# Kernel optimization log

Measured on AMD Instinct MI355X. Metric: run time of the kernel, lower is better.

The kernel has to match this reference:

```python
import jax, jax.numpy as jnp
import numpy as np

ACT_BITS = 8  # config.activation_bits
HIDDEN = 2048
INTERMEDIATE = 4096  # hidden * mlp_ratio (2.0), power of 2
EPS = 1e-5


def fwht(x):
    """Normalized fast Walsh-Hadamard transform along last axis (n = power of 2)."""
    shape = x.shape
    n = shape[-1]
    x = x.reshape(-1, n)
    h = 1
    while h < n:  # log2(n) fixed iterations, not a data-dim loop
        x = x.reshape(-1, n // (2 * h), 2, h)
        a, b = x[:, :, 0, :], x[:, :, 1, :]
        x = jnp.stack((a + b, a - b), axis=2).reshape(-1, n)
        h *= 2
    return (x * (1.0 / np.sqrt(n))).reshape(shape)


def _ste(x, q):
    # straight-through estimator: forward uses q, backward passes grad to x
    return x + jax.lax.stop_gradient(q - x)


def act_quant(x, bits):
    """Per-token absmax quantization to `bits` bits (BitNet a8 style), dequantized."""
    qb = float(2 ** (bits - 1) - 1)
    scale = qb / jnp.clip(jnp.max(jnp.abs(x), axis=-1, keepdims=True), EPS, None)
    q = jnp.clip(jnp.round(x * scale), -qb, qb) / scale
    return _ste(x, q)


def weight_quant(w):
    """Ternary absmean weight quantization (BitNet b1.58), dequantized."""
    scale = jnp.clip(jnp.mean(jnp.abs(w)), EPS, None)
    q = jnp.clip(jnp.round(w / scale), -1.0, 1.0) * scale
    return _ste(w, q)


def hbitlinear(x, w, bits):
    # H-BitLinear: Hadamard-rotate activations, quantize acts + weights, GEMM
    xq = act_quant(fwht(x), bits)
    wq = weight_quant(w)
    return jnp.einsum('bsd,fd->bsf', xq, wq)


def setup_inputs() -> dict:
    key = jax.random.key(0)
    k1, k2, k3 = jax.random.split(key, 3)
    hidden_states = jax.random.normal(k1, (4, 4096, HIDDEN), dtype=jnp.float32)
    w_up = jax.random.normal(k2, (INTERMEDIATE, HIDDEN), dtype=jnp.float32) * 0.02
    w_down = jax.random.normal(k3, (HIDDEN, INTERMEDIATE), dtype=jnp.float32) * 0.02
    return {"hidden_states": hidden_states, "w_up": w_up, "w_down": w_down}


def reference(hidden_states, w_up, w_down):
    h = hbitlinear(hidden_states, w_up, ACT_BITS)      # (B, S, intermediate)
    h = jnp.square(jax.nn.relu(h))                     # squared ReLU
    # dropout p=0.0 -> identity in eval/reference
    return hbitlinear(h, w_down, ACT_BITS)             # (B, S, hidden)
```

## Files before the change

### kernel.cpp

```cpp
#include <hip/hip_runtime.h>
#include <hip/hip_fp16.h>
#include <cstdint>
#include <cstddef>

#define HIDDEN 2048
#define INTER  4096
#define EPSQ   1e-5f

typedef int v4i __attribute__((ext_vector_type(4)));

__device__ __forceinline__ void async_ld16(const void* g, void* l) {
  __builtin_amdgcn_global_load_lds((const __attribute__((address_space(1))) void*)g,
                                   (__attribute__((address_space(3))) void*)l, 16, 0, 0);
}

#define BAR()   __builtin_amdgcn_s_barrier()
#define VMC(n)  asm volatile("s_waitcnt vmcnt(" #n ")" ::: "memory")

__global__ void absmean_kernel(const float* __restrict__ w, size_t n4, double* __restrict__ out) {
  double s = 0.0;
  const float4* w4 = (const float4*)w;
  for (size_t i = blockIdx.x * (size_t)blockDim.x + threadIdx.x; i < n4;
       i += (size_t)gridDim.x * blockDim.x) {
    float4 v = w4[i];
    s += (double)fabsf(v.x) + (double)fabsf(v.y) + (double)fabsf(v.z) + (double)fabsf(v.w);
  }
  #pragma unroll
  for (int o = 32; o; o >>= 1) s += __shfl_down(s, o);
  __shared__ double red[4];
  if ((threadIdx.x & 63) == 0) red[threadIdx.x >> 6] = s;
  __syncthreads();
  if (threadIdx.x == 0) atomicAdd(out, red[0] + red[1] + red[2] + red[3]);
}

__global__ void quantw_kernel(const float* __restrict__ w, size_t n4,
                              const double* __restrict__ sum, double invcnt,
                              int8_t* __restrict__ q) {
  const float scale = (float)fmax(sum[0] * invcnt, (double)EPSQ);
  const float4* w4 = (const float4*)w;
  char4* q4 = (char4*)q;
  for (size_t i = blockIdx.x * (size_t)blockDim.x + threadIdx.x; i < n4;
       i += (size_t)gridDim.x * blockDim.x) {
    float4 v = w4[i];
    char4 c;
    c.x = (signed char)fmaxf(-1.f, fminf(1.f, rintf(v.x / scale)));
    c.y = (signed char)fmaxf(-1.f, fminf(1.f, rintf(v.y / scale)));
    c.z = (signed char)fmaxf(-1.f, fminf(1.f, rintf(v.z / scale)));
    c.w = (signed char)fmaxf(-1.f, fminf(1.f, rintf(v.w / scale)));
    q4[i] = c;
  }
}

template <int LOGN, bool HALF_IN>
__global__ void __launch_bounds__(256) fwht_quant_kernel(const void* __restrict__ Xv,
                                                         int8_t* __restrict__ Q,
                                                         float* __restrict__ invs) {
  constexpr int N = 1 << LOGN;
  constexpr int E = N / 64;
  const int lane = threadIdx.x & 63;
  const size_t t = (size_t)blockIdx.x * 4 + (threadIdx.x >> 6);

  float r[E];
  if constexpr (HALF_IN) {
    const int4* xp = (const int4*)((const __half*)Xv + t * (size_t)N + lane * E);
    #pragma unroll
    for (int u = 0; u < E / 8; ++u) {
      alignas(16) __half hb[8];
      *(int4*)hb = xp[u];
      #pragma unroll
      for (int j = 0; j < 8; ++j) r[u * 8 + j] = __half2float(hb[j]);
    }
  } else {
    const float4* xp = (const float4*)((const float*)Xv + t * (size_t)N + lane * E);
    #pragma unroll
    for (int u = 0; u < E / 4; ++u) {
      float4 v = xp[u];
      r[u * 4 + 0] = v.x; r[u * 4 + 1] = v.y; r[u * 4 + 2] = v.z; r[u * 4 + 3] = v.w;
    }
  }

  #pragma unroll
  for (int m = 1; m < E; m <<= 1) {
    #pragma unroll
    for (int e = 0; e < E; ++e) {
      if (!(e & m)) {
        float a = r[e], b = r[e | m];
        r[e] = a + b;
        r[e | m] = a - b;
      }
    }
  }
  #pragma unroll
  for (int m = 1; m < 64; m <<= 1) {
    const float sgn = (lane & m) ? -1.f : 1.f;
    #pragma unroll
    for (int e = 0; e < E; ++e) {
      float w = __shfl_xor(r[e], m, 64);
      r[e] = fmaf(r[e], sgn, w);
    }
  }

  float mx = 0.f;
  #pragma unroll
  for (int e = 0; e < E; ++e) mx = fmaxf(mx, fabsf(r[e]));
  #pragma unroll
  for (int m = 1; m < 64; m <<= 1) mx = fmaxf(mx, __shfl_xor(mx, m, 64));

  constexpr float c = (LOGN == 11) ? 0.022097086912079608f : 0.015625f;
  mx = fmaxf(mx * c, EPSQ);
  const float sc = 127.0f * c / mx;
  if (lane == 0) invs[t] = mx * (1.0f / 127.0f);

  alignas(16) int8_t qv[E];
  #pragma unroll
  for (int e = 0; e < E; ++e) {
    float q = rintf(r[e] * sc);
    q = fmaxf(-127.f, fminf(127.f, q));
    qv[e] = (int8_t)q;
  }
  int8_t* qp = Q + t * (size_t)N + lane * E;
  #pragma unroll
  for (int u = 0; u < E / 16; ++u) ((int4*)qp)[u] = ((const int4*)qv)[u];
}

template <bool RELU2, typename TOUT>
__global__ __launch_bounds__(512, 2)
void gemm_i8_8ph(const int8_t* __restrict__ A, const int8_t* __restrict__ B,
                 TOUT* __restrict__ C, const float* __restrict__ invs,
                 const double* __restrict__ wsum, double invcnt,
                 int N, int K) {
  __shared__ int8_t As[2 * 2 * 128 * 128];
  __shared__ int8_t Bs[2 * 2 * 128 * 128];

  const int GX = N >> 8;
  const int nwg = gridDim.x;
  int wg = blockIdx.x;
  wg = (wg & 7) * (nwg >> 3) + (wg >> 3);
  const int bx = wg % GX;
  const int by = wg / GX;
  const int m0 = by * 256, n0 = bx * 256;

  const int t = threadIdx.x;
  const int lane = t & 63;
  const int wave = t >> 6;
  const int wr = wave >> 2;
  const int wc = wave & 3;

  const int row0 = t >> 3;
  const int colsw = ((t & 7) * 16) ^ ((row0 & 7) << 4);
  const int8_t* gA0 = A + (size_t)(m0 + row0) * K + colsw;
  const int8_t* gA1 = gA0 + (size_t)128 * K;
  const int8_t* gB0 = B + (size_t)(n0 + row0) * K + colsw;
  const int8_t* gB1 = gB0 + (size_t)128 * K;
  const size_t rstep = (size_t)64 * K;

  auto SA = [&](int bf, int hf, int kt) {
    const int8_t* g = (hf ? gA1 : gA0) + (size_t)kt * 128;
    int8_t* l = As + bf * 32768 + hf * 16384 + t * 16;
    async_ld16(g, l);
    async_ld16(g + rstep, l + 8192);
  };
  auto SB = [&](int bf, int hf, int kt) {
    const int8_t* g = (hf ? gB1 : gB0) + (size_t)kt * 128;
    int8_t* l = Bs + bf * 32768 + hf * 16384 + t * 16;
    async_ld16(g, l);
    async_ld16(g + rstep, l + 8192);
  };

  const int csw0 = ((lane >> 4) * 16) ^ ((lane & 7) << 4);
  const int csw1 = (64 + (lane >> 4) * 16) ^ ((lane & 7) << 4);
  const int8_t* pA0 = As + wr * 16384 + (lane & 15) * 128;
  const int8_t* pB0 = Bs + (wc >> 1) * 16384 + ((wc & 1) * 64 + (lane & 15)) * 128;

  v4i acc[8][4] = {};
  v4i a[4][2], b[4][2];

  auto RDA = [&](int bf, int m4) {
    const int8_t* p = pA0 + bf * 32768 + m4 * 8192;
    #pragma unroll
    for (int mt = 0; mt < 4; ++mt) {
      a[mt][0] = *(const v4i*)(p + mt * 2048 + csw0);
      a[mt][1] = *(const v4i*)(p + mt * 2048 + csw1);
    }
  };
  auto RDB = [&](int bf, int n2) {
    const int8_t* p = pB0 + bf * 32768 + n2 * 4096;
    #pragma unroll
    for (int nt = 0; nt < 2; ++nt) {
      b[n2 * 2 + nt][0] = *(const v4i*)(p + nt * 2048 + csw0);
      b[n2 * 2 + nt][1] = *(const v4i*)(p + nt * 2048 + csw1);
    }
  };
  auto MM = [&](int m4, int n2) {
    __builtin_amdgcn_s_setprio(1);
    #pragma unroll
    for (int mt = 0; mt < 4; ++mt)
      #pragma unroll
      for (int nt = 0; nt < 2; ++nt) {
        v4i* c = &acc[m4 * 4 + mt][n2 * 2 + nt];
        *c = __builtin_amdgcn_mfma_i32_16x16x64_i8(a[mt][0], b[n2 * 2 + nt][0], *c, 0, 0, 0);
        *c = __builtin_amdgcn_mfma_i32_16x16x64_i8(a[mt][1], b[n2 * 2 + nt][1], *c, 0, 0, 0);
      }
    __builtin_amdgcn_s_setprio(0);
  };

  const int NIT = K >> 8;

  SB(0, 0, 0); SB(0, 1, 0); SA(0, 0, 0); SA(0, 1, 0);
  SB(1, 0, 1); SB(1, 1, 1); SA(1, 0, 1); SA(1, 1, 1);
  VMC(8);
  BAR();

  for (int it = 0; it < NIT; ++it) {
    const int kt2 = 2 * it + 2, kt3 = 2 * it + 3;
    const bool more = it < NIT - 1;

    RDA(0, 0); RDB(0, 0);
    BAR(); MM(0, 0); BAR();

    RDB(0, 1);
    BAR(); MM(0, 1); BAR();

    RDA(0, 1);
    if (more) { SB(0, 0, kt2); SB(0, 1, kt2); }
    BAR(); MM(1, 0); BAR();

    if (more) { SA(0, 0, kt2); SA(0, 1, kt2); VMC(8); } else { VMC(0); }
    BAR(); MM(1, 1); BAR();

    RDA(1, 0); RDB(1, 0);
    BAR(); MM(0, 0); BAR();

    RDB(1, 1);
    BAR(); MM(0, 1); BAR();

    RDA(1, 1);
    if (more) { SB(1, 0, kt3); SB(1, 1, kt3); }
    BAR(); MM(1, 0); BAR();

    if (more) { SA(1, 0, kt3); SA(1, 1, kt3); VMC(8); }
    BAR(); MM(1, 1); BAR();
  }

  const float wscale = (float)fmax(wsum[0] * invcnt, (double)EPSQ);
  const int crow_base = m0 + wr * 128 + (lane >> 4) * 4;
  const int ccol_base = n0 + wc * 64 + (lane & 15);
  #pragma unroll
  for (int mt = 0; mt < 8; ++mt) {
    const int trow = crow_base + mt * 16;
    float fr[4];
    #pragma unroll
    for (int r = 0; r < 4; ++r) fr[r] = wscale * invs[trow + r];
    #pragma unroll
    for (int nt = 0; nt < 4; ++nt) {
      const int col = ccol_base + nt * 16;
      #pragma unroll
      for (int r = 0; r < 4; ++r) {
        float v = (float)acc[mt][nt][r] * fr[r];
        if (RELU2) v = v > 0.f ? v * v : 0.f;
        if constexpr (sizeof(TOUT) == 2)
          C[(size_t)(trow + r) * N + col] = __float2half(v);
        else
          C[(size_t)(trow + r) * N + col] = v;
      }
    }
  }
}

extern "C" void kernel_launch(void* const* d_in, const int* in_sizes, int n_in,
                              void* d_out, int out_size, void* d_ws, size_t ws_size,
                              hipStream_t stream) {
  const float* x      = (const float*)d_in[0];
  const float* w_up   = (const float*)d_in[1];
  const float* w_down = (const float*)d_in[2];
  float* out = (float*)d_out;

  const int T = in_sizes[0] / HIDDEN;
  const size_t WN = (size_t)INTER * HIDDEN;

  char* ws = (char*)d_ws;
  double* sums   = (double*)ws;
  float* invs1   = (float*)(ws + 256);
  float* invs2   = (float*)(ws + 256 + 65536);
  int8_t* wq_up  = (int8_t*)(ws + 131328);
  int8_t* wq_dn  = wq_up + WN;
  int8_t* a8_1   = wq_dn + WN;
  int8_t* a8_2   = a8_1 + (size_t)T * HIDDEN;
  __half* h      = (__half*)(a8_2 + (size_t)T * INTER);

  const double invcnt = 1.0 / (double)WN;

  hipMemsetAsync(sums, 0, 256, stream);
  absmean_kernel<<<1024, 256, 0, stream>>>(w_up, WN / 4, sums + 0);
  absmean_kernel<<<1024, 256, 0, stream>>>(w_down, WN / 4, sums + 1);
  quantw_kernel<<<2048, 256, 0, stream>>>(w_up, WN / 4, sums + 0, invcnt, wq_up);
  quantw_kernel<<<2048, 256, 0, stream>>>(w_down, WN / 4, sums + 1, invcnt, wq_dn);

  fwht_quant_kernel<11, false><<<T / 4, 256, 0, stream>>>(x, a8_1, invs1);
  gemm_i8_8ph<true, __half><<<(T / 256) * (INTER / 256), 512, 0, stream>>>(
      a8_1, wq_up, h, invs1, sums + 0, invcnt, INTER, HIDDEN);
  fwht_quant_kernel<12, true><<<T / 4, 256, 0, stream>>>(h, a8_2, invs2);
  gemm_i8_8ph<false, float><<<(T / 256) * (HIDDEN / 256), 512, 0, stream>>>(
      a8_2, wq_dn, out, invs2, sums + 1, invcnt, HIDDEN, INTER);
}
```

Measured before the change: 654.8 us.

## Software-pipeline LDS fragment reads with ping-pong registers and fewer barriers in int8 GEMM

```diff
diff --git a/kernel.cpp b/kernel.cpp
--- a/kernel.cpp
+++ b/kernel.cpp
@@ -173,34 +173,28 @@
   const int8_t* pB0 = Bs + (wc >> 1) * 16384 + ((wc & 1) * 64 + (lane & 15)) * 128;
 
   v4i acc[8][4] = {};
-  v4i a[4][2], b[4][2];
-
-  auto RDA = [&](int bf, int m4) {
+  v4i aA[4], aB[4], bA[2], bB[2];
+
+  auto RDa = [&](v4i (&af)[4], int bf, int m4, int kk) {
     const int8_t* p = pA0 + bf * 32768 + m4 * 8192;
-    #pragma unroll
-    for (int mt = 0; mt < 4; ++mt) {
-      a[mt][0] = *(const v4i*)(p + mt * 2048 + csw0);
-      a[mt][1] = *(const v4i*)(p + mt * 2048 + csw1);
-    }
-  };
-  auto RDB = [&](int bf, int n2) {
-    const int8_t* p = pB0 + bf * 32768 + n2 * 4096;
-    #pragma unroll
-    for (int nt = 0; nt < 2; ++nt) {
-      b[n2 * 2 + nt][0] = *(const v4i*)(p + nt * 2048 + csw0);
-      b[n2 * 2 + nt][1] = *(const v4i*)(p + nt * 2048 + csw1);
-    }
-  };
-  auto MM = [&](int m4, int n2) {
+    const int cs = kk ? csw1 : csw0;
+    #pragma unroll
+    for (int mt = 0; mt < 4; ++mt) af[mt] = *(const v4i*)(p + mt * 2048 + cs);
+  };
+  auto RDb = [&](v4i (&bf)[2], int buf, int n2, int kk) {
+    const int8_t* p = pB0 + buf * 32768 + n2 * 4096;
+    const int cs = kk ? csw1 : csw0;
+    #pragma unroll
+    for (int nt = 0; nt < 2; ++nt) bf[nt] = *(const v4i*)(p + nt * 2048 + cs);
+  };
+  auto MMC = [&](int m4, int n2, v4i (&af)[4], v4i (&bf)[2]) {
     __builtin_amdgcn_s_setprio(1);
     #pragma unroll
     for (int mt = 0; mt < 4; ++mt)
       #pragma unroll
-      for (int nt = 0; nt < 2; ++nt) {
-        v4i* c = &acc[m4 * 4 + mt][n2 * 2 + nt];
-        *c = __builtin_amdgcn_mfma_i32_16x16x64_i8(a[mt][0], b[n2 * 2 + nt][0], *c, 0, 0, 0);
-        *c = __builtin_amdgcn_mfma_i32_16x16x64_i8(a[mt][1], b[n2 * 2 + nt][1], *c, 0, 0, 0);
-      }
+      for (int nt = 0; nt < 2; ++nt)
+        acc[m4 * 4 + mt][n2 * 2 + nt] =
+            __builtin_amdgcn_mfma_i32_16x16x64_i8(af[mt], bf[nt], acc[m4 * 4 + mt][n2 * 2 + nt], 0, 0, 0);
     __builtin_amdgcn_s_setprio(0);
   };
 
@@ -210,36 +204,40 @@
   SB(1, 0, 1); SB(1, 1, 1); SA(1, 0, 1); SA(1, 1, 1);
   VMC(8);
   BAR();
+  RDa(aA, 0, 0, 0); RDb(bA, 0, 0, 0);
 
   for (int it = 0; it < NIT; ++it) {
     const int kt2 = 2 * it + 2, kt3 = 2 * it + 3;
     const bool more = it < NIT - 1;
 
-    RDA(0, 0); RDB(0, 0);
-    BAR(); MM(0, 0); BAR();
-
-    RDB(0, 1);
-    BAR(); MM(0, 1); BAR();
-
-    RDA(0, 1);
+    RDb(bB, 0, 1, 0);                       MMC(0, 0, aA, bA);
+    RDa(aB, 0, 1, 0);                       MMC(0, 1, aA, bB);
+                                            MMC(1, 1, aB, bB);
+    RDa(aA, 0, 1, 1); RDb(bB, 0, 0, 1);     MMC(1, 0, aB, bA);
+    RDb(bA, 0, 1, 1);                       MMC(1, 0, aA, bB);
+    RDa(aB, 0, 0, 1);                       MMC(1, 1, aA, bA);
+    BAR();
     if (more) { SB(0, 0, kt2); SB(0, 1, kt2); }
-    BAR(); MM(1, 0); BAR();
-
+                                            MMC(0, 1, aB, bA);
+    BAR();
     if (more) { SA(0, 0, kt2); SA(0, 1, kt2); VMC(8); } else { VMC(0); }
-    BAR(); MM(1, 1); BAR();
-
-    RDA(1, 0); RDB(1, 0);
-    BAR(); MM(0, 0); BAR();
-
-    RDB(1, 1);
-    BAR(); MM(0, 1); BAR();
-
-    RDA(1, 1);
+    BAR();
+    RDa(aA, 1, 0, 0); RDb(bA, 1, 0, 0);     MMC(0, 0, aB, bB);
+
+    RDb(bB, 1, 1, 0);                       MMC(0, 0, aA, bA);
+    RDa(aB, 1, 1, 0);                       MMC(0, 1, aA, bB);
+                                            MMC(1, 1, aB, bB);
+    RDa(aA, 1, 1, 1); RDb(bB, 1, 0, 1);     MMC(1, 0, aB, bA);
+    RDb(bA, 1, 1, 1);                       MMC(1, 0, aA, bB);
+    RDa(aB, 1, 0, 1);                       MMC(1, 1, aA, bA);
+    BAR();
     if (more) { SB(1, 0, kt3); SB(1, 1, kt3); }
-    BAR(); MM(1, 0); BAR();
-
-    if (more) { SA(1, 0, kt3); SA(1, 1, kt3); VMC(8); }
-    BAR(); MM(1, 1); BAR();
+                                            MMC(0, 1, aB, bA);
+    BAR();
+    if (more) { SA(1, 0, kt3); SA(1, 1, kt3); VMC(8); } else { VMC(0); }
+    BAR();
+    if (more) { RDa(aA, 0, 0, 0); RDb(bA, 0, 0, 0); }
+                                            MMC(0, 0, aB, bB);
   }
 
   const float wscale = (float)fmax(wsum[0] * invcnt, (double)EPSQ);
```

New measurement: 683.1 us. 1.04x slower.
